# Performance work log

Hardware: AMD Instinct MI355X
Metric: run time of the kernel (lower is better)

The kernel has to match this reference:

```python
import jax, jax.numpy as jnp
import numpy as np

P = 0.9  # CLOP swap probability (init kwarg)


def _index_permute(key, n_element, dim):
    """Faithful port of CLOPLayer._index_permute: sequential conditional
    neighbor swaps over a flat index array, expressed as a lax.scan.
    Swap choices r in {0..4} with probs (1-p/2, p/8, p/8, p/8, p/8);
    r maps to offset {0, +1, -1, +dim, -dim}; swap only if r!=0 and
    0 < idx < n_element (strict >0, matching the original code)."""
    probs = jnp.array([1.0 - P / 2, P / 8, P / 8, P / 8, P / 8], dtype=jnp.float32)
    # loop runs i over abs(range(-n+1, n)) -> 2n-1 steps
    iters = jnp.abs(jnp.arange(-n_element + 1, n_element, dtype=jnp.int32))
    rs = jax.random.choice(key, 5, shape=(iters.shape[0],), p=probs)
    offsets = jnp.array([0, 1, -1, dim, -dim], dtype=jnp.int32)

    def step(perm, inp):
        i, r = inp
        idx = i + offsets[r]
        do = (r != 0) & (idx > 0) & (idx < n_element)
        idx_c = jnp.clip(idx, 0, n_element - 1)
        a = perm[i]
        b = perm[idx_c]
        # conditional swap; when do is False both writes restore originals
        perm = perm.at[i].set(jnp.where(do, b, a))
        perm = perm.at[idx_c].set(jnp.where(do, a, b))
        return perm, None

    perm0 = jnp.arange(n_element, dtype=jnp.int32)
    perm, _ = jax.lax.scan(step, perm0, (iters, rs))
    return perm


def setup_inputs() -> dict:
    key = jax.random.key(0)
    x = jax.random.normal(key, (512, 9, 84, 84), dtype=jnp.float32)
    return {"x": x}


def reference(x):
    B, C, H, W = x.shape
    n = H * W  # n_element of x[0,0]; dim = int(sqrt(n)) == H for square images
    perm = _index_permute(jax.random.key(42), n, H)
    flat = x.reshape(B, C, n)
    # torch.gather(flat, 2, idx) with idx broadcast over (B, C)
    res = jnp.take(flat, perm, axis=2)
    return res.reshape(x.shape)
```

## Files before the change

kernel.cpp:

```cpp
#include <hip/hip_runtime.h>

#define N_ELEM   7056
#define DIM      84
#define M_STEPS  14111
#define N_ROWS   4608
#define NCHUNK   384
#define KSTEPS   37
#define WINW     208
#define TPB      256
#define NJV      1764

__device__ __forceinline__ void threefry2x32(unsigned k0, unsigned k1,
                                             unsigned x0, unsigned x1,
                                             unsigned &o0, unsigned &o1) {
  const unsigned ks0 = k0, ks1 = k1, ks2 = k0 ^ k1 ^ 0x1BD11BDAu;
  x0 += ks0; x1 += ks1;
#define ROTL(x, r) (((x) << (r)) | ((x) >> (32 - (r))))
#define RND(r) { x0 += x1; x1 = ROTL(x1, r); x1 ^= x0; }
  RND(13) RND(15) RND(26) RND(6)
  x0 += ks1; x1 += ks2 + 1u;
  RND(17) RND(29) RND(16) RND(24)
  x0 += ks2; x1 += ks0 + 2u;
  RND(13) RND(15) RND(26) RND(6)
  x0 += ks0; x1 += ks1 + 3u;
  RND(17) RND(29) RND(16) RND(24)
  x0 += ks1; x1 += ks2 + 4u;
  RND(13) RND(15) RND(26) RND(6)
  x0 += ks2; x1 += ks0 + 5u;
  o0 = x0; o1 = x1;
#undef RND
#undef ROTL
}

__device__ __forceinline__ int r_from_bits(unsigned bits) {
  const float p8 = 0.1125f;
  const float q0 = 0.55f;
  const float q1 = q0 + p8;
  const float q2 = q1 + p8;
  const float q3 = q2 + p8;
  const float q4 = q3 + p8;
  float u  = __uint_as_float((bits >> 9) | 0x3F800000u) - 1.0f;
  float rv = q4 * (1.0f - u);
  return (int)(q0 < rv) + (int)(q1 < rv) + (int)(q2 < rv) + (int)(q3 < rv);
}

__device__ __forceinline__ void chunk_bounds(int c, int &t0, int &t1, int &lo, int &hi) {
  t0 = c * KSTEPS; if (t0 > M_STEPS) t0 = M_STEPS;
  t1 = t0 + KSTEPS; if (t1 > M_STEPS) t1 = M_STEPS;
  int a0 = t0 - (N_ELEM - 1);       if (a0 < 0) a0 = -a0;
  int a1 = (t1 - 1) - (N_ELEM - 1); if (a1 < 0) a1 = -a1;
  int imax = a0 > a1 ? a0 : a1;
  int imin;
  if (t0 <= N_ELEM - 1 && t1 - 1 >= N_ELEM - 1) imin = 0;
  else imin = a0 < a1 ? a0 : a1;
  lo = imin - DIM; if (lo < 0) lo = 0;
  hi = imax + DIM; if (hi > N_ELEM - 1) hi = N_ELEM - 1;
}

__global__ __launch_bounds__(TPB) void chunk_kernel(unsigned* __restrict__ winG) {
  __shared__ __align__(16) unsigned short w[WINW];
  __shared__ unsigned char rs[KSTEPS + 3];

  const int c = blockIdx.x, tid = threadIdx.x;
  int t0, t1, lo, hi; chunk_bounds(c, t0, t1, lo, hi);
  const int nt = t1 - t0;

  if (tid < WINW) w[tid] = (unsigned short)(lo + tid);
  if (tid < nt) {
    unsigned y0, y1;
    threefry2x32(0u, 42u, 0u, (unsigned)(t0 + tid), y0, y1);
    rs[tid] = (unsigned char)r_from_bits(y0 ^ y1);
  }
  __syncthreads();

  if (tid == 0) {
    for (int k = 0; k < nt; ++k) {
      int t = t0 + k;
      int i = t - (N_ELEM - 1); if (i < 0) i = -i;
      int r = rs[k];
      int off = (r == 1) ? 1 : (r == 2) ? -1 : (r == 3) ? DIM : (r == 4) ? -DIM : 0;
      int idx = i + off;
      bool doit = (r != 0) && (idx > 0) && (idx < N_ELEM);
      int je = doit ? idx : i;
      unsigned short a = w[i  - lo];
      unsigned short b = w[je - lo];
      w[i  - lo] = b;
      w[je - lo] = a;
    }
  }
  __syncthreads();

  const uint4* w4 = (const uint4*)w;
  if (tid < WINW * 2 / 16) ((uint4*)winG)[c * (WINW * 2 / 16) + tid] = w4[tid];
}

#define TRACE_BLOCKS 28
#define WPP 128
__global__ __launch_bounds__(TPB) void trace_kernel(const unsigned* __restrict__ winG,
                                                    int* __restrict__ permG) {
  __shared__ __align__(16) unsigned short w[WPP * WINW];
  const int tid = threadIdx.x;
  const int U4_PER_WIN = WINW * 2 / 16;

  int y = blockIdx.x * 252 + tid;

  for (int pass = NCHUNK / WPP - 1; pass >= 0; --pass) {
    const int cbase = pass * WPP;
    uint4* w4 = (uint4*)w;
    const uint4* g4 = (const uint4*)winG + cbase * U4_PER_WIN;
    for (int k = tid; k < WPP * U4_PER_WIN; k += TPB) w4[k] = g4[k];
    __syncthreads();

    if (tid < 252) {
      for (int c = WPP - 1; c >= 0; --c) {
        int t0, t1, lo, hi; chunk_bounds(cbase + c, t0, t1, lo, hi);
        unsigned e = (unsigned)(y - lo);
        if (e <= (unsigned)(hi - lo)) y = (int)w[c * WINW + e];
      }
    }
    __syncthreads();
  }

  if (tid < 252) permG[blockIdx.x * 252 + tid] = y;
}

__global__ __launch_bounds__(TPB) void gather_kernel(const float* __restrict__ x,
                                                     const int* __restrict__ perm,
                                                     float* __restrict__ out) {
  __shared__ __align__(16) float row[N_ELEM];
  const int r = blockIdx.x;
  const int tid = threadIdx.x;

  const float4* xr4 = (const float4*)(x + (size_t)r * N_ELEM);
  float4* row4 = (float4*)row;
  for (int v = tid; v < NJV; v += TPB) row4[v] = xr4[v];
  __syncthreads();

  float4* or4 = (float4*)(out + (size_t)r * N_ELEM);
  const int4* p4 = (const int4*)perm;
  for (int v = tid; v < NJV; v += TPB) {
    int4 p = p4[v];
    float4 o;
    o.x = row[p.x]; o.y = row[p.y]; o.z = row[p.z]; o.w = row[p.w];
    or4[v] = o;
  }
}

extern "C" void kernel_launch(void* const* d_in, const int* in_sizes, int n_in,
                              void* d_out, int out_size, void* d_ws, size_t ws_size,
                              hipStream_t stream) {
  const float* x = (const float*)d_in[0];
  float* out = (float*)d_out;

  unsigned* winG = (unsigned*)d_ws;
  int* perm = (int*)((char*)d_ws + NCHUNK * WINW * 2);

  chunk_kernel<<<NCHUNK, TPB, 0, stream>>>(winG);
  trace_kernel<<<TRACE_BLOCKS, TPB, 0, stream>>>(winG, perm);
  gather_kernel<<<N_ROWS, TPB, 0, stream>>>(x, perm, out);
}
```

Baseline: 268.0 us.

## Gather directly from global memory with perm cached in LDS across nine rows

The gather kernel no longer stages each row in shared memory. It converts the permutation to 16-bit indices in LDS once per block, then gathers directly from global memory for nine rows per block. Outputs are written with nontemporal stores. This amortizes the permutation load, cuts LDS traffic and syncs, and launches fewer blocks. The cost is that reads become scattered global loads that depend on cache locality, since the permutation swaps only neighbouring elements.

```diff
diff --git a/kernel.cpp b/kernel.cpp
--- a/kernel.cpp
+++ b/kernel.cpp
@@ -9,6 +9,9 @@
 #define WINW     208
 #define TPB      256
 #define NJV      1764
+#define GR       9
+
+typedef float f4 __attribute__((ext_vector_type(4)));
 
 __device__ __forceinline__ void threefry2x32(unsigned k0, unsigned k1,
                                              unsigned x0, unsigned x1,
@@ -127,22 +130,32 @@
 __global__ __launch_bounds__(TPB) void gather_kernel(const float* __restrict__ x,
                                                      const int* __restrict__ perm,
                                                      float* __restrict__ out) {
-  __shared__ __align__(16) float row[N_ELEM];
-  const int r = blockIdx.x;
+  __shared__ __align__(16) unsigned short p16[N_ELEM];
   const int tid = threadIdx.x;
 
-  const float4* xr4 = (const float4*)(x + (size_t)r * N_ELEM);
-  float4* row4 = (float4*)row;
-  for (int v = tid; v < NJV; v += TPB) row4[v] = xr4[v];
+  const int4* pi4 = (const int4*)perm;
+  for (int v = tid; v < NJV; v += TPB) {
+    int4 p = pi4[v];
+    ushort4 s;
+    s.x = (unsigned short)p.x; s.y = (unsigned short)p.y;
+    s.z = (unsigned short)p.z; s.w = (unsigned short)p.w;
+    ((ushort4*)p16)[v] = s;
+  }
   __syncthreads();
 
-  float4* or4 = (float4*)(out + (size_t)r * N_ELEM);
-  const int4* p4 = (const int4*)perm;
+  const size_t base = (size_t)blockIdx.x * GR * N_ELEM;
+  const float* xb = x + base;
+  float*       ob = out + base;
+
   for (int v = tid; v < NJV; v += TPB) {
-    int4 p = p4[v];
-    float4 o;
-    o.x = row[p.x]; o.y = row[p.y]; o.z = row[p.z]; o.w = row[p.w];
-    or4[v] = o;
+    ushort4 p = ((const ushort4*)p16)[v];
+#pragma unroll
+    for (int rr = 0; rr < GR; ++rr) {
+      const float* xr = xb + rr * N_ELEM;
+      f4 o;
+      o.x = xr[p.x]; o.y = xr[p.y]; o.z = xr[p.z]; o.w = xr[p.w];
+      __builtin_nontemporal_store(o, (f4*)(ob + rr * N_ELEM) + v);
+    }
   }
 }
 
@@ -157,5 +170,5 @@
 
   chunk_kernel<<<NCHUNK, TPB, 0, stream>>>(winG);
   trace_kernel<<<TRACE_BLOCKS, TPB, 0, stream>>>(winG, perm);
-  gather_kernel<<<N_ROWS, TPB, 0, stream>>>(x, perm, out);
+  gather_kernel<<<N_ROWS / GR, TPB, 0, stream>>>(x, perm, out);
 }
```

Result: slower. 279.9 us (+4.4%).
